# Performance work log

Measured on AMD Instinct MI355X. Metric: run time of the kernel, lower is better.

The kernel has to match this reference:

```python
import jax, jax.numpy as jnp
import numpy as np

B, L, K, T, C_IN, C_OUT, TKS = 32, 1855, 7, 40, 8, 32, 5


def setup_inputs() -> dict:
    key = jax.random.key(0)
    k1, k2, k3, k4 = jax.random.split(key, 4)
    x = jax.random.normal(k1, (B, L, T, C_IN), dtype=jnp.float32)
    idx = jax.random.randint(k2, (L, K), 0, L, dtype=jnp.int32)
    missing = jax.random.uniform(k3, (L, K)) < 0.1
    neighbor_indices = jnp.where(missing, jnp.int32(-1), idx)
    fan_in = K * TKS * C_IN
    fan_out = K * TKS * C_OUT
    limit = np.sqrt(6.0 / (fan_in + fan_out))  # glorot uniform
    kernel = jax.random.uniform(k4, (K, TKS, C_IN, C_OUT), dtype=jnp.float32,
                                minval=-limit, maxval=limit)
    bias = jnp.zeros((C_OUT,), dtype=jnp.float32)
    return {"x": x, "neighbor_indices": neighbor_indices, "kernel": kernel, "bias": bias}


def reference(x, neighbor_indices, kernel, bias):
    # x: (B, L, T, C_in); neighbor_indices: (L, K) with -1 = missing
    mask = (neighbor_indices != -1)
    safe_idx = jnp.where(mask, neighbor_indices, 0)
    # gather neighbor features: (B, L, K, T, C_in)
    nf = x[:, safe_idx]
    nf = nf * mask[None, :, :, None, None].astype(x.dtype)
    tks = kernel.shape[1]
    t_out = x.shape[2] - tks + 1
    # valid temporal conv: sum over small fixed tau instead of materializing
    # the (B, L, K, T_out, tks, C_in) framed tensor
    out = jnp.zeros((x.shape[0], x.shape[1], t_out, kernel.shape[-1]), dtype=x.dtype)
    for tau in range(tks):
        out = out + jnp.einsum('blkti,kio->blto',
                               nf[:, :, :, tau:tau + t_out, :], kernel[:, tau])
    return out + bias
```

## Files before the change

kernel.cpp:

```cpp
#include <hip/hip_runtime.h>

constexpr int Bn = 32, Ln = 1855, Kn = 7, Tn = 40, CIn = 8, COn = 32, TKSn = 5, TOn = 36;
constexpr int BG   = 8;
constexpr int KRED = Kn * TKSn * CIn;
constexpr int KPAD = 288;
constexpr int WROW = 296;
constexpr int XS_ELEMS = BG * Kn * Tn * CIn;
constexpr int XB  = 2;
constexpr int XS3 = XB * Kn * Tn * CIn;
constexpr size_t XN = (size_t)Bn * Ln * Tn * CIn;

constexpr size_t WS_WT   = 0;
constexpr size_t WS_ZPAD = 18432;
constexpr size_t WS_XBF  = 18560;
constexpr size_t WS_NEED = WS_XBF + XN * 2;

typedef __attribute__((ext_vector_type(8))) short bf16x8;
typedef __attribute__((ext_vector_type(8))) unsigned short u16x8;
typedef __attribute__((ext_vector_type(4))) float f32x4;

__device__ inline unsigned short f2bf(float f) {
    unsigned u = __builtin_bit_cast(unsigned, f);
    u += 0x7fffu + ((u >> 16) & 1u);
    return (unsigned short)(u >> 16);
}

__device__ inline void gload_lds16(const void* g, void* lds) {
    __builtin_amdgcn_global_load_lds(
        (const __attribute__((address_space(1))) unsigned int*)g,
        (__attribute__((address_space(3))) unsigned int*)lds,
        16, 0, 0);
}

__global__ __launch_bounds__(256) void prep_all(const float* __restrict__ x,
                                                unsigned short* __restrict__ xbf,
                                                const float* __restrict__ w,
                                                unsigned short* __restrict__ wt,
                                                unsigned short* __restrict__ zpad) {
    const int tid = threadIdx.x;
    if (blockIdx.x == 2048) {
        for (int p = tid; p < KRED * COn; p += 256) {
            int o  = p & 31;
            int kr = p >> 5;
            wt[o * KPAD + kr] = f2bf(w[p]);
        }
        for (int p = tid; p < COn * (KPAD - KRED); p += 256) {
            int o = p >> 3;
            wt[o * KPAD + KRED + (p & 7)] = 0;
        }
        if (tid < 64) zpad[tid] = 0;
        return;
    }
    const size_t n8 = XN / 8;
    for (size_t p = (size_t)blockIdx.x * 256 + tid; p < n8; p += (size_t)2048 * 256) {
        float4 a = ((const float4*)x)[2 * p];
        float4 b = ((const float4*)x)[2 * p + 1];
        u16x8 v;
        v[0] = f2bf(a.x); v[1] = f2bf(a.y); v[2] = f2bf(a.z); v[3] = f2bf(a.w);
        v[4] = f2bf(b.x); v[5] = f2bf(b.y); v[6] = f2bf(b.z); v[7] = f2bf(b.w);
        *(u16x8*)&xbf[p * 8] = v;
    }
}

template<int RT0, int NT, bool TAIL>
__device__ __forceinline__ void do_tiles6(
    const unsigned short* __restrict__ xs,
    const bf16x8 (&bfrag)[2][9], float bv0, float bv1,
    float* __restrict__ out, int b0, int l, int quad, int lrow)
{
    f32x4 acc[NT][2];
    int base[NT];
    #pragma unroll
    for (int i = 0; i < NT; ++i) {
        acc[i][0] = f32x4{0.f,0.f,0.f,0.f};
        acc[i][1] = f32x4{0.f,0.f,0.f,0.f};
        int m;
        if (TAIL && i == NT - 1) m = 64 + (lrow & 7);
        else                     m = (RT0 + i) * 16 + lrow;
        const int bl = m / 36, t = m - bl * 36;
        base[i] = bl * 2240 + t * 8;
    }
    __builtin_amdgcn_s_setprio(1);
    #pragma unroll
    for (int c = 0; c < 9; ++c) {
        const int p = c * 4 + quad;
        const int knbr = p / 5, tau = p - knbr * 5;
        const int koff = knbr * 320 + tau * 8;
        #pragma unroll
        for (int i = 0; i < NT; ++i) {
            int o = base[i] + koff;
            if (c == 8 && quad == 3) o = XS3;
            bf16x8 a = *(const bf16x8*)&xs[o];
            acc[i][0] = __builtin_amdgcn_mfma_f32_16x16x32_bf16(a, bfrag[0][c], acc[i][0], 0, 0, 0);
            acc[i][1] = __builtin_amdgcn_mfma_f32_16x16x32_bf16(a, bfrag[1][c], acc[i][1], 0, 0, 0);
        }
    }
    __builtin_amdgcn_s_setprio(0);
    #pragma unroll
    for (int i = 0; i < NT; ++i) {
        const bool tail_tile = TAIL && (i == NT - 1);
        if (tail_tile && quad >= 2) continue;
        #pragma unroll
        for (int reg = 0; reg < 4; ++reg) {
            const int m  = (RT0 + i) * 16 + quad * 4 + reg;
            const int bl = m / 36, t = m - bl * 36;
            const size_t off =
                (((size_t)(b0 + bl) * Ln + l) * TOn + t) * COn + lrow;
            __builtin_nontemporal_store(acc[i][0][reg] + bv0, &out[off]);
            __builtin_nontemporal_store(acc[i][1][reg] + bv1, &out[off + 16]);
        }
    }
}

__global__ __launch_bounds__(64, 3) void conv_mfma6(
    const unsigned short* __restrict__ xbf,
    const int*   __restrict__ nbr,
    const unsigned short* __restrict__ wt,
    const unsigned short* __restrict__ zpad,
    const float* __restrict__ bias,
    float*       __restrict__ out)
{
    __shared__ unsigned short xs[XS3 + 8];

    const int lane = threadIdx.x;
    const int l    = blockIdx.x;
    const int b0   = blockIdx.y * XB;

    if (lane < 8) xs[XS3 + lane] = 0;

    int nv = 0;
    if (lane < Kn) nv = nbr[l * Kn + lane];

    #pragma unroll
    for (int s = 0; s < 9; ++s) {
        if (s < 8 || lane < 48) {
            const int u   = s * 64 + lane;
            const int row = u / 40;
            const int q   = u - row * 40;
            const int bl  = row / 7;
            const int k   = row - bl * 7;
            const int l2  = __shfl(nv, k);
            const unsigned short* src = zpad;
            if (l2 >= 0)
                src = xbf + ((size_t)(b0 + bl) * Ln + l2) * 320 + q * 8;
            gload_lds16(src, &xs[s * 512]);
        }
    }

    const int quad = lane >> 4;
    const int lrow = lane & 15;

    bf16x8 bfrag[2][9];
    #pragma unroll
    for (int oh = 0; oh < 2; ++oh)
        #pragma unroll
        for (int c = 0; c < 9; ++c)
            bfrag[oh][c] = *(const bf16x8*)(wt + (oh * 16 + lrow) * KPAD + c * 32 + quad * 8);
    const float bv0 = bias[lrow];
    const float bv1 = bias[16 + lrow];

    asm volatile("s_waitcnt vmcnt(0)" ::: "memory");

    do_tiles6<0, 3, false>(xs, bfrag, bv0, bv1, out, b0, l, quad, lrow);
    do_tiles6<3, 2, true >(xs, bfrag, bv0, bv1, out, b0, l, quad, lrow);
}

__global__ __launch_bounds__(256) void conv_mfma(
    const float* __restrict__ x, const int* __restrict__ nbr,
    const float* __restrict__ w, const float* __restrict__ bias,
    float* __restrict__ out)
{
    __shared__ unsigned short xs[XS_ELEMS + 8];
    __shared__ unsigned short wt[COn * WROW];

    const int tid = threadIdx.x;
    const int l   = blockIdx.x;
    const int bg  = blockIdx.y;

    for (int p = tid; p < KRED * COn; p += 256) {
        int o  = p & 31;
        int kr = p >> 5;
        wt[o * WROW + kr] = f2bf(w[p]);
    }
    for (int p = tid; p < COn * (WROW - KRED); p += 256) {
        int o = p >> 4;
        wt[o * WROW + KRED + (p & 15)] = 0;
    }
    if (tid < 8) xs[XS_ELEMS + tid] = 0;

    for (int p = tid; p < BG * Kn * 80; p += 256) {
        int b_local = p / 560;
        int r = p - b_local * 560;
        int k = r / 80;
        int q = r - k * 80;
        int l2 = nbr[l * Kn + k];
        float4 v = make_float4(0.f, 0.f, 0.f, 0.f);
        if (l2 >= 0)
            v = ((const float4*)x)[((size_t)(bg * BG + b_local) * Ln + l2) * 80 + q];
        ushort4 pk;
        pk.x = f2bf(v.x); pk.y = f2bf(v.y); pk.z = f2bf(v.z); pk.w = f2bf(v.w);
        *(ushort4*)&xs[p * 4] = pk;
    }
    __syncthreads();

    const int wave = tid >> 6;
    const int lane = tid & 63;
    const int quad = lane >> 4;
    const int lrow = lane & 15;
    const int o_base  = (wave & 1) * 16;
    const int rt_base = (wave >> 1) * 9;

    bf16x8 bfrag[9];
    #pragma unroll
    for (int c = 0; c < 9; ++c)
        bfrag[c] = *(const bf16x8*)&wt[(o_base + lrow) * WROW + c * 32 + quad * 8];

    const float bv = bias[o_base + lrow];

    #pragma unroll
    for (int g = 0; g < 3; ++g) {
        const int rt0 = rt_base + g * 3;
        f32x4 acc0 = {0.f,0.f,0.f,0.f}, acc1 = acc0, acc2 = acc0;
        const int m0 = (rt0 + 0) * 16 + lrow;
        const int m1 = (rt0 + 1) * 16 + lrow;
        const int m2 = (rt0 + 2) * 16 + lrow;
        const int bl0 = m0 / 36, t0 = m0 - bl0 * 36;
        const int bl1 = m1 / 36, t1 = m1 - bl1 * 36;
        const int bl2 = m2 / 36, t2 = m2 - bl2 * 36;
        const int base0 = bl0 * 2240 + t0 * 8;
        const int base1 = bl1 * 2240 + t1 * 8;
        const int base2 = bl2 * 2240 + t2 * 8;
        #pragma unroll
        for (int c = 0; c < 9; ++c) {
            const int p = c * 4 + quad;
            const int knbr = p / 5, tau = p - knbr * 5;
            const int koff = knbr * 320 + tau * 8;
            int o0 = base0 + koff, o1 = base1 + koff, o2 = base2 + koff;
            if (c == 8 && quad == 3) { o0 = XS_ELEMS; o1 = XS_ELEMS; o2 = XS_ELEMS; }
            bf16x8 a0 = *(const bf16x8*)&xs[o0];
            bf16x8 a1 = *(const bf16x8*)&xs[o1];
            bf16x8 a2 = *(const bf16x8*)&xs[o2];
            acc0 = __builtin_amdgcn_mfma_f32_16x16x32_bf16(a0, bfrag[c], acc0, 0, 0, 0);
            acc1 = __builtin_amdgcn_mfma_f32_16x16x32_bf16(a1, bfrag[c], acc1, 0, 0, 0);
            acc2 = __builtin_amdgcn_mfma_f32_16x16x32_bf16(a2, bfrag[c], acc2, 0, 0, 0);
        }
        #pragma unroll
        for (int i = 0; i < 3; ++i) {
            const f32x4 acc = (i == 0) ? acc0 : ((i == 1) ? acc1 : acc2);
            const int rt = rt0 + i;
            #pragma unroll
            for (int reg = 0; reg < 4; ++reg) {
                const int m  = rt * 16 + quad * 4 + reg;
                const int bl = m / 36, t = m - bl * 36;
                const size_t off =
                    (((size_t)(bg * BG + bl) * Ln + l) * TOn + t) * COn + o_base + lrow;
                out[off] = acc[reg] + bv;
            }
        }
    }
}

extern "C" void kernel_launch(void* const* d_in, const int* in_sizes, int n_in,
                              void* d_out, int out_size, void* d_ws, size_t ws_size,
                              hipStream_t stream) {
    const float* x    = (const float*)d_in[0];
    const int*   nbr  = (const int*)d_in[1];
    const float* w    = (const float*)d_in[2];
    const float* bias = (const float*)d_in[3];
    float*       out  = (float*)d_out;

    if (ws_size >= WS_NEED && d_ws != nullptr) {
        unsigned short* wt   = (unsigned short*)((char*)d_ws + WS_WT);
        unsigned short* zpad = (unsigned short*)((char*)d_ws + WS_ZPAD);
        unsigned short* xbf  = (unsigned short*)((char*)d_ws + WS_XBF);
        prep_all<<<2049, 256, 0, stream>>>(x, xbf, w, wt, zpad);
        conv_mfma6<<<dim3(Ln, Bn / XB), dim3(64), 0, stream>>>(xbf, nbr, wt, zpad, bias, out);
    } else {
        conv_mfma<<<dim3(Ln, Bn / BG), dim3(256), 0, stream>>>(x, nbr, w, bias, out);
    }
}
```

Measured before the change: 363.4 us.

## Read gathered neighbor rows directly from global memory instead of staging in LDS

The conv kernel no longer stages the gathered neighbor slices into shared memory with global_load_lds. Each MFMA A-fragment is now loaded straight from the bf16 copy of x, using per-chunk byte offsets computed from the neighbor indices. Missing neighbors and the padding chunk point at a zero row placed after xbf in the workspace. This removes the LDS staging step and its wait barrier. In exchange, every fragment becomes a scattered global load that relies on L1/L2 reuse, adds latency inside the MFMA loop, and uses 32-bit byte offsets into a large buffer.

```diff
diff --git a/kernel.cpp b/kernel.cpp
--- a/kernel.cpp
+++ b/kernel.cpp
@@ -7,13 +7,13 @@
 constexpr int WROW = 296;
 constexpr int XS_ELEMS = BG * Kn * Tn * CIn;
 constexpr int XB  = 2;
-constexpr int XS3 = XB * Kn * Tn * CIn;
 constexpr size_t XN = (size_t)Bn * Ln * Tn * CIn;
 
 constexpr size_t WS_WT   = 0;
-constexpr size_t WS_ZPAD = 18432;
 constexpr size_t WS_XBF  = 18560;
-constexpr size_t WS_NEED = WS_XBF + XN * 2;
+constexpr size_t WS_ZROW = WS_XBF + XN * 2;
+constexpr size_t WS_NEED = WS_ZROW + 128;
+constexpr unsigned ZOFF_U = (unsigned)(XN * 2);
 
 typedef __attribute__((ext_vector_type(8))) short bf16x8;
 typedef __attribute__((ext_vector_type(8))) unsigned short u16x8;
@@ -25,18 +25,11 @@
     return (unsigned short)(u >> 16);
 }
 
-__device__ inline void gload_lds16(const void* g, void* lds) {
-    __builtin_amdgcn_global_load_lds(
-        (const __attribute__((address_space(1))) unsigned int*)g,
-        (__attribute__((address_space(3))) unsigned int*)lds,
-        16, 0, 0);
-}
-
 __global__ __launch_bounds__(256) void prep_all(const float* __restrict__ x,
                                                 unsigned short* __restrict__ xbf,
                                                 const float* __restrict__ w,
                                                 unsigned short* __restrict__ wt,
-                                                unsigned short* __restrict__ zpad) {
+                                                unsigned short* __restrict__ zrow) {
     const int tid = threadIdx.x;
     if (blockIdx.x == 2048) {
         for (int p = tid; p < KRED * COn; p += 256) {
@@ -48,7 +41,7 @@
             int o = p >> 3;
             wt[o * KPAD + KRED + (p & 7)] = 0;
         }
-        if (tid < 64) zpad[tid] = 0;
+        if (tid < 64) zrow[tid] = 0;
         return;
     }
     const size_t n8 = XN / 8;
@@ -63,13 +56,14 @@
 }
 
 template<int RT0, int NT, bool TAIL>
-__device__ __forceinline__ void do_tiles6(
-    const unsigned short* __restrict__ xs,
+__device__ __forceinline__ void do_tiles7(
+    const char* __restrict__ xb,
+    const unsigned (&voff)[9], const bool (&vld)[9],
     const bf16x8 (&bfrag)[2][9], float bv0, float bv1,
     float* __restrict__ out, int b0, int l, int quad, int lrow)
 {
     f32x4 acc[NT][2];
-    int base[NT];
+    unsigned soffv[NT];
     #pragma unroll
     for (int i = 0; i < NT; ++i) {
         acc[i][0] = f32x4{0.f,0.f,0.f,0.f};
@@ -78,19 +72,15 @@
         if (TAIL && i == NT - 1) m = 64 + (lrow & 7);
         else                     m = (RT0 + i) * 16 + lrow;
         const int bl = m / 36, t = m - bl * 36;
-        base[i] = bl * 2240 + t * 8;
+        soffv[i] = (unsigned)((b0 + bl) * Ln) * 640u + (unsigned)t * 16u;
     }
     __builtin_amdgcn_s_setprio(1);
     #pragma unroll
     for (int c = 0; c < 9; ++c) {
-        const int p = c * 4 + quad;
-        const int knbr = p / 5, tau = p - knbr * 5;
-        const int koff = knbr * 320 + tau * 8;
         #pragma unroll
         for (int i = 0; i < NT; ++i) {
-            int o = base[i] + koff;
-            if (c == 8 && quad == 3) o = XS3;
-            bf16x8 a = *(const bf16x8*)&xs[o];
+            const unsigned vo = vld[c] ? (soffv[i] + voff[c]) : ZOFF_U;
+            bf16x8 a = *(const bf16x8*)(xb + vo);
             acc[i][0] = __builtin_amdgcn_mfma_f32_16x16x32_bf16(a, bfrag[0][c], acc[i][0], 0, 0, 0);
             acc[i][1] = __builtin_amdgcn_mfma_f32_16x16x32_bf16(a, bfrag[1][c], acc[i][1], 0, 0, 0);
         }
@@ -112,43 +102,33 @@
     }
 }
 
-__global__ __launch_bounds__(64, 3) void conv_mfma6(
+__global__ __launch_bounds__(64, 3) void conv_mfma7(
     const unsigned short* __restrict__ xbf,
     const int*   __restrict__ nbr,
     const unsigned short* __restrict__ wt,
-    const unsigned short* __restrict__ zpad,
     const float* __restrict__ bias,
     float*       __restrict__ out)
 {
-    __shared__ unsigned short xs[XS3 + 8];
-
     const int lane = threadIdx.x;
     const int l    = blockIdx.x;
     const int b0   = blockIdx.y * XB;
 
-    if (lane < 8) xs[XS3 + lane] = 0;
-
     int nv = 0;
     if (lane < Kn) nv = nbr[l * Kn + lane];
 
-    #pragma unroll
-    for (int s = 0; s < 9; ++s) {
-        if (s < 8 || lane < 48) {
-            const int u   = s * 64 + lane;
-            const int row = u / 40;
-            const int q   = u - row * 40;
-            const int bl  = row / 7;
-            const int k   = row - bl * 7;
-            const int l2  = __shfl(nv, k);
-            const unsigned short* src = zpad;
-            if (l2 >= 0)
-                src = xbf + ((size_t)(b0 + bl) * Ln + l2) * 320 + q * 8;
-            gload_lds16(src, &xs[s * 512]);
-        }
-    }
-
     const int quad = lane >> 4;
     const int lrow = lane & 15;
+
+    unsigned voff[9]; bool vld[9];
+    #pragma unroll
+    for (int c = 0; c < 9; ++c) {
+        const int p   = c * 4 + quad;
+        const int kk  = p / 5;
+        const int tau = p - kk * 5;
+        const int l2  = __shfl(nv, (p >= 35) ? 0 : kk);
+        vld[c]  = (p < 35) && (l2 >= 0);
+        voff[c] = (unsigned)l2 * 640u + (unsigned)tau * 16u;
+    }
 
     bf16x8 bfrag[2][9];
     #pragma unroll
@@ -159,10 +139,10 @@
     const float bv0 = bias[lrow];
     const float bv1 = bias[16 + lrow];
 
-    asm volatile("s_waitcnt vmcnt(0)" ::: "memory");
-
-    do_tiles6<0, 3, false>(xs, bfrag, bv0, bv1, out, b0, l, quad, lrow);
-    do_tiles6<3, 2, true >(xs, bfrag, bv0, bv1, out, b0, l, quad, lrow);
+    const char* xb = (const char*)xbf;
+
+    do_tiles7<0, 3, false>(xb, voff, vld, bfrag, bv0, bv1, out, b0, l, quad, lrow);
+    do_tiles7<3, 2, true >(xb, voff, vld, bfrag, bv0, bv1, out, b0, l, quad, lrow);
 }
 
 __global__ __launch_bounds__(256) void conv_mfma(
@@ -271,10 +251,10 @@
 
     if (ws_size >= WS_NEED && d_ws != nullptr) {
         unsigned short* wt   = (unsigned short*)((char*)d_ws + WS_WT);
-        unsigned short* zpad = (unsigned short*)((char*)d_ws + WS_ZPAD);
         unsigned short* xbf  = (unsigned short*)((char*)d_ws + WS_XBF);
-        prep_all<<<2049, 256, 0, stream>>>(x, xbf, w, wt, zpad);
-        conv_mfma6<<<dim3(Ln, Bn / XB), dim3(64), 0, stream>>>(xbf, nbr, wt, zpad, bias, out);
+        unsigned short* zrow = (unsigned short*)((char*)d_ws + WS_ZROW);
+        prep_all<<<2049, 256, 0, stream>>>(x, xbf, w, wt, zrow);
+        conv_mfma7<<<dim3(Ln, Bn / XB), dim3(64), 0, stream>>>(xbf, nbr, wt, bias, out);
     } else {
         conv_mfma<<<dim3(Ln, Bn / BG), dim3(256), 0, stream>>>(x, nbr, w, bias, out);
     }
```

Result: slower. 409.8 us (+12.7%).
